# Performance work log

Hardware: AMD Instinct MI355X
Metric: run time of the kernel (lower is better)

Reference implementation:

```python
import jax, jax.numpy as jnp
import numpy as np

QUERY_DIM = 256
HIDDEN_DIM = 256
NUM_HEADS = 8
HEAD_DIM = HIDDEN_DIM // NUM_HEADS
NORM_FACT = float(HIDDEN_DIM / NUM_HEADS) ** (-0.5)


def setup_inputs() -> dict:
    key = jax.random.key(0)
    ks = jax.random.split(key, 7)
    b, Q, H, W = 4, 300, 100, 100
    q = jax.random.normal(ks[0], (b, Q, QUERY_DIM), dtype=jnp.float32)
    k = jax.random.normal(ks[1], (b, QUERY_DIM, H, W), dtype=jnp.float32)
    mask = jax.random.randint(ks[2], (b, H, W), 0, 2).astype(jnp.bool_)
    # xavier_uniform for Linear(query_dim, hidden_dim): bound = sqrt(6/(fan_in+fan_out))
    bound = float(np.sqrt(6.0 / (QUERY_DIM + HIDDEN_DIM)))
    q_w = jax.random.uniform(ks[3], (HIDDEN_DIM, QUERY_DIM), jnp.float32, -bound, bound)
    k_w = jax.random.uniform(ks[4], (HIDDEN_DIM, QUERY_DIM), jnp.float32, -bound, bound)
    q_b = jnp.zeros((HIDDEN_DIM,), jnp.float32)
    k_b = jnp.zeros((HIDDEN_DIM,), jnp.float32)
    return {"q": q, "k": k, "mask": mask, "q_w": q_w, "q_b": q_b, "k_w": k_w, "k_b": k_b}


def reference(q, k, mask, q_w, q_b, k_w, k_b):
    b, Q, _ = q.shape
    _, C, H, W = k.shape
    # q_linear: [b,Q,query_dim] -> [b,Q,hidden]
    qp = jnp.einsum('bqc,hc->bqh', q, q_w) + q_b
    # k projection: 1x1 conv == channel-wise linear: [b,C,H,W] -> [b,hidden,H,W]
    kp = jnp.einsum('bchw,oc->bohw', k, k_w) + k_b[None, :, None, None]
    qh = qp.reshape(b, Q, NUM_HEADS, HEAD_DIM)
    kh = kp.reshape(b, NUM_HEADS, HEAD_DIM, H, W)
    # attention scores: [b, Q, n_heads, H, W]
    weights = jnp.einsum('bqnc,bnchw->bqnhw', qh * NORM_FACT, kh)
    if mask is not None:
        weights = jnp.where(mask[:, None, None, :, :], -jnp.inf, weights)
    # softmax over flattened (heads, H, W) — faithful to flatten(2) in the original
    flat = weights.reshape(b, Q, NUM_HEADS * H * W)
    weights = jax.nn.softmax(flat, axis=-1).reshape(b, Q, NUM_HEADS, H, W)
    return weights
```

## Files before the change

### kernel.cpp

```cpp
#include <hip/hip_runtime.h>
#include <math.h>

#define BB 4
#define QQ 300
#define CC 256
#define NH 8
#define HD 32
#define HWN 10000
#define NT 625
#define NCHUNK 125
#define TPC 5
#define MT 19
#define NORM_FACT 0.17677669529663687f

typedef __attribute__((ext_vector_type(8))) short short8_t;
typedef __attribute__((ext_vector_type(4))) float f32x4_t;
typedef __attribute__((ext_vector_type(4))) int   i32x4_t;

union FragU { uint32_t u[4]; short8_t v; };

__device__ __forceinline__ unsigned short bf16_rn(float x) {
    uint32_t u = __float_as_uint(x);
    return (unsigned short)((u + 0x7fffu + ((u >> 16) & 1u)) >> 16);
}
__device__ __forceinline__ float bf16_f(unsigned short h) {
    return __uint_as_float(((uint32_t)h) << 16);
}

__global__ void prep_kwB_kernel(const float* __restrict__ kw,
                                unsigned short* __restrict__ kwB_hi,
                                unsigned short* __restrict__ kwB_lo) {
    const int ot = blockIdx.x, ks = blockIdx.y;
    const int l = threadIdx.x;
    const int o = ot * 16 + (l & 15);
    const int c0 = ks * 32 + (l >> 4) * 8;
    const size_t base = ((size_t)(ot * 8 + ks) * 64 + l) * 8;
    #pragma unroll
    for (int j = 0; j < 8; ++j) {
        const float x = kw[o * CC + c0 + j];
        const unsigned short h = bf16_rn(x);
        kwB_hi[base + j] = h;
        kwB_lo[base + j] = bf16_rn(x - bf16_f(h));
    }
}

__global__ void qproj_kernel(const float* __restrict__ q,
                             const float* __restrict__ qw,
                             const float* __restrict__ qb,
                             unsigned short* __restrict__ qp_il) {
    __shared__ float qrow[CC];
    const int bq = blockIdx.x;
    const int h  = threadIdx.x;
    qrow[h] = q[bq * CC + h];
    __syncthreads();
    float acc = qb[h];
    const float* wr = qw + h * CC;
    #pragma unroll 4
    for (int c = 0; c < CC; c += 4) {
        float4 w = *reinterpret_cast<const float4*>(wr + c);
        float4 x = *reinterpret_cast<const float4*>(&qrow[c]);
        acc += w.x * x.x + w.y * x.y + w.z * x.z + w.w * x.w;
    }
    acc *= NORM_FACT;
    const unsigned short hi = bf16_rn(acc);
    const size_t base = ((size_t)bq * NH + (h >> 5)) * 64 + (h & 31);
    qp_il[base]      = hi;
    qp_il[base + 32] = bf16_rn(acc - bf16_f(hi));
}

__global__ __launch_bounds__(256)
void kproj_kernel(const float* __restrict__ kin,
                  const unsigned short* __restrict__ kwB_hi,
                  const unsigned short* __restrict__ kwB_lo,
                  const float* __restrict__ kb,
                  unsigned short* __restrict__ kp_il) {
    const int wid = threadIdx.x >> 6, l = threadIdx.x & 63;
    const int wu  = blockIdx.x * 4 + wid;
    const int ot4 = wu & 3;
    const int rem = wu >> 2;
    const int hwt = rem % NT;
    const int b   = rem / NT;
    const int hw  = hwt * 16 + (l & 15);
    const int jb  = (l >> 4) * 8;

    f32x4_t acc[4];
    #pragma unroll
    for (int t = 0; t < 4; ++t) {
        const float bias = kb[(ot4 * 4 + t) * 16 + (l & 15)];
        acc[t] = {bias, bias, bias, bias};
    }

    const float* kbase = kin + (size_t)b * CC * HWN + hw;
    #pragma unroll 2
    for (int ks = 0; ks < 8; ++ks) {
        FragU a_hi, a_lo;
        #pragma unroll
        for (int tt = 0; tt < 4; ++tt) {
            const int c = ks * 32 + jb + 2 * tt;
            const float x0 = kbase[(size_t)c * HWN];
            const float x1 = kbase[(size_t)(c + 1) * HWN];
            const unsigned short h0 = bf16_rn(x0), h1 = bf16_rn(x1);
            const unsigned short g0 = bf16_rn(x0 - bf16_f(h0));
            const unsigned short g1 = bf16_rn(x1 - bf16_f(h1));
            a_hi.u[tt] = (uint32_t)h0 | ((uint32_t)h1 << 16);
            a_lo.u[tt] = (uint32_t)g0 | ((uint32_t)g1 << 16);
        }
        #pragma unroll
        for (int t = 0; t < 4; ++t) {
            const int ot = ot4 * 4 + t;
            const size_t fb = ((size_t)(ot * 8 + ks) * 64 + l) * 8;
            const short8_t bh = *reinterpret_cast<const short8_t*>(kwB_hi + fb);
            const short8_t bl = *reinterpret_cast<const short8_t*>(kwB_lo + fb);
            acc[t] = __builtin_amdgcn_mfma_f32_16x16x32_bf16(a_hi.v, bh, acc[t], 0, 0, 0);
            acc[t] = __builtin_amdgcn_mfma_f32_16x16x32_bf16(a_hi.v, bl, acc[t], 0, 0, 0);
            acc[t] = __builtin_amdgcn_mfma_f32_16x16x32_bf16(a_lo.v, bh, acc[t], 0, 0, 0);
        }
    }

    #pragma unroll
    for (int t = 0; t < 4; ++t) {
        const int o = (ot4 * 4 + t) * 16 + (l & 15);
        const int n = o >> 5, osub = o & 31;
        #pragma unroll
        for (int r = 0; r < 4; ++r) {
            const int hwrow = hwt * 16 + (l >> 4) * 4 + r;
            const size_t base = ((size_t)(b * HWN + hwrow) * NH + n) * 64 + osub;
            const float v = acc[t][r];
            const unsigned short h = bf16_rn(v);
            kp_il[base]      = h;
            kp_il[base + 32] = bf16_rn(v - bf16_f(h));
        }
    }
}

__global__ __launch_bounds__(256)
void attn_stats_kernel(const unsigned short* __restrict__ qp_il,
                       const unsigned short* __restrict__ kp_il,
                       const int* __restrict__ mask,
                       float* __restrict__ partials) {
    const int wid = threadIdx.x >> 6, l = threadIdx.x & 63;
    const int wu = blockIdx.x * 4 + wid;
    const int ch = wu % NCHUNK;
    int tmp = wu / NCHUNK;
    const int n = tmp & 7;
    const int b = tmp >> 3;

    short8_t ah[TPC], al[TPC];
    float mf[TPC][4];
    #pragma unroll
    for (int t = 0; t < TPC; ++t) {
        const int tile = ch * TPC + t;
        const int hwr = tile * 16 + (l & 15);
        const size_t abase = ((size_t)(b * HWN + hwr) * NH + n) * 64 + (l >> 4) * 8;
        ah[t] = *reinterpret_cast<const short8_t*>(kp_il + abase);
        al[t] = *reinterpret_cast<const short8_t*>(kp_il + abase + 32);
        const int hw4 = tile * 16 + (l >> 4) * 4;
        const i32x4_t mv = *reinterpret_cast<const i32x4_t*>(mask + b * HWN + hw4);
        mf[t][0] = mv.x ? 0.f : 1.f;
        mf[t][1] = mv.y ? 0.f : 1.f;
        mf[t][2] = mv.z ? 0.f : 1.f;
        mf[t][3] = mv.w ? 0.f : 1.f;
    }

    const size_t qslice = ((size_t)b * QQ) * NH + n;
    #pragma unroll 2
    for (int qt = 0; qt < MT; ++qt) {
        const int qa = qt * 16 + (l & 15);
        const int qcl = qa < QQ ? qa : QQ - 1;
        const size_t bbase = ((size_t)(b * QQ + qcl) * NH + n) * 64 + (l >> 4) * 8;
        const short8_t bh = *reinterpret_cast<const short8_t*>(qp_il + bbase);
        const short8_t bl = *reinterpret_cast<const short8_t*>(qp_il + bbase + 32);

        float a = 0.f;
        #pragma unroll
        for (int t = 0; t < TPC; ++t) {
            f32x4_t c = {0.f, 0.f, 0.f, 0.f};
            c = __builtin_amdgcn_mfma_f32_16x16x32_bf16(ah[t], bh, c, 0, 0, 0);
            c = __builtin_amdgcn_mfma_f32_16x16x32_bf16(ah[t], bl, c, 0, 0, 0);
            c = __builtin_amdgcn_mfma_f32_16x16x32_bf16(al[t], bh, c, 0, 0, 0);
            a += __expf(c[0]) * mf[t][0] + __expf(c[1]) * mf[t][1]
               + __expf(c[2]) * mf[t][2] + __expf(c[3]) * mf[t][3];
        }
        a += __shfl_xor(a, 16, 64);
        a += __shfl_xor(a, 32, 64);
        if (l < 16) {
            const int qr = qt * 16 + l;
            if (qr < QQ)
                partials[(((size_t)b * QQ + qr) * NH + n) * NCHUNK + ch] = a;
        }
    }
    (void)qslice;
}

__global__ void invsum_kernel(const float* __restrict__ partials,
                              float* __restrict__ invS) {
    const int row = blockIdx.x;
    const int l = threadIdx.x;
    float s = 0.f;
    const float* p = partials + (size_t)row * (NH * NCHUNK);
    for (int i = l; i < NH * NCHUNK; i += 64) s += p[i];
    #pragma unroll
    for (int m = 1; m < 64; m <<= 1) s += __shfl_xor(s, m, 64);
    if (l == 0) invS[row] = 1.0f / s;
}

__global__ __launch_bounds__(256)
void attn_out_kernel(const unsigned short* __restrict__ qp_il,
                     const unsigned short* __restrict__ kp_il,
                     const int* __restrict__ mask,
                     const float* __restrict__ invS,
                     float* __restrict__ out) {
    const int wid = threadIdx.x >> 6, l = threadIdx.x & 63;
    const int wu = blockIdx.x * 4 + wid;
    const int ch = wu % NCHUNK;
    int tmp = wu / NCHUNK;
    const int n = tmp & 7;
    const int b = tmp >> 3;

    short8_t ah[TPC], al[TPC];
    float mf[TPC][4];
    int hw4v[TPC];
    #pragma unroll
    for (int t = 0; t < TPC; ++t) {
        const int tile = ch * TPC + t;
        const int hwr = tile * 16 + (l & 15);
        const size_t abase = ((size_t)(b * HWN + hwr) * NH + n) * 64 + (l >> 4) * 8;
        ah[t] = *reinterpret_cast<const short8_t*>(kp_il + abase);
        al[t] = *reinterpret_cast<const short8_t*>(kp_il + abase + 32);
        const int hw4 = tile * 16 + (l >> 4) * 4;
        hw4v[t] = hw4;
        const i32x4_t mv = *reinterpret_cast<const i32x4_t*>(mask + b * HWN + hw4);
        mf[t][0] = mv.x ? 0.f : 1.f;
        mf[t][1] = mv.y ? 0.f : 1.f;
        mf[t][2] = mv.z ? 0.f : 1.f;
        mf[t][3] = mv.w ? 0.f : 1.f;
    }

    #pragma unroll 2
    for (int qt = 0; qt < MT; ++qt) {
        const int qa = qt * 16 + (l & 15);
        const int qcl = qa < QQ ? qa : QQ - 1;
        const bool qok = qa < QQ;
        const size_t bbase = ((size_t)(b * QQ + qcl) * NH + n) * 64 + (l >> 4) * 8;
        const short8_t bh = *reinterpret_cast<const short8_t*>(qp_il + bbase);
        const short8_t bl = *reinterpret_cast<const short8_t*>(qp_il + bbase + 32);
        const float is = invS[b * QQ + qcl];
        float* const obase = out + (((size_t)b * QQ + qcl) * NH + n) * HWN;

        #pragma unroll
        for (int t = 0; t < TPC; ++t) {
            f32x4_t c = {0.f, 0.f, 0.f, 0.f};
            c = __builtin_amdgcn_mfma_f32_16x16x32_bf16(ah[t], bh, c, 0, 0, 0);
            c = __builtin_amdgcn_mfma_f32_16x16x32_bf16(ah[t], bl, c, 0, 0, 0);
            c = __builtin_amdgcn_mfma_f32_16x16x32_bf16(al[t], bh, c, 0, 0, 0);
            f32x4_t rv;
            rv[0] = __expf(c[0]) * is * mf[t][0];
            rv[1] = __expf(c[1]) * is * mf[t][1];
            rv[2] = __expf(c[2]) * is * mf[t][2];
            rv[3] = __expf(c[3]) * is * mf[t][3];
            if (qok)
                __builtin_nontemporal_store(rv,
                    reinterpret_cast<f32x4_t*>(obase + hw4v[t]));
        }
    }
}

extern "C" void kernel_launch(void* const* d_in, const int* in_sizes, int n_in,
                              void* d_out, int out_size, void* d_ws, size_t ws_size,
                              hipStream_t stream) {
    const float* q    = (const float*)d_in[0];
    const float* k    = (const float*)d_in[1];
    const int*   mask = (const int*)d_in[2];
    const float* qw   = (const float*)d_in[3];
    const float* qb   = (const float*)d_in[4];
    const float* kw   = (const float*)d_in[5];
    const float* kb   = (const float*)d_in[6];
    float* out = (float*)d_out;

    char* wsb = (char*)d_ws;
    unsigned short* kp_il = (unsigned short*)wsb;
    unsigned short* qp_il = (unsigned short*)(wsb + 40960000);
    float* invS           = (float*)(wsb + 40960000 + 1228800);

    unsigned short* kwB_hi = (unsigned short*)d_out;
    unsigned short* kwB_lo = kwB_hi + 65536;
    float* partials = (float*)((char*)d_out + (4u << 20));

    prep_kwB_kernel<<<dim3(16, 8), 64, 0, stream>>>(kw, kwB_hi, kwB_lo);
    qproj_kernel<<<BB * QQ, 256, 0, stream>>>(q, qw, qb, qp_il);
    kproj_kernel<<<(BB * NT * 4) / 4, 256, 0, stream>>>(k, kwB_hi, kwB_lo, kb, kp_il);
    attn_stats_kernel<<<(BB * NH * NCHUNK) / 4, 256, 0, stream>>>(
        qp_il, kp_il, mask, partials);
    invsum_kernel<<<BB * QQ, 64, 0, stream>>>(partials, invS);
    attn_out_kernel<<<(BB * NH * NCHUNK) / 4, 256, 0, stream>>>(
        qp_il, kp_il, mask, invS, out);
}
```

Baseline: 249.0 us.

## Stage k tile in shared memory for kproj and split Q tiles across two waves

```diff
diff --git a/kernel.cpp b/kernel.cpp
--- a/kernel.cpp
+++ b/kernel.cpp
@@ -74,31 +74,48 @@
                   const unsigned short* __restrict__ kwB_lo,
                   const float* __restrict__ kb,
                   unsigned short* __restrict__ kp_il) {
+    __shared__ float kf[CC][17];
     const int wid = threadIdx.x >> 6, l = threadIdx.x & 63;
-    const int wu  = blockIdx.x * 4 + wid;
-    const int ot4 = wu & 3;
-    const int rem = wu >> 2;
-    const int hwt = rem % NT;
-    const int b   = rem / NT;
-    const int hw  = hwt * 16 + (l & 15);
+    const int bu  = blockIdx.x;
+    const int hwt = bu % NT;
+    const int b   = bu / NT;
+    const int ot4 = wid;
+
+    {
+        const int tid = threadIdx.x;
+        const float* kb0 = kin + (size_t)b * CC * HWN + hwt * 16;
+        #pragma unroll
+        for (int iter = 0; iter < 4; ++iter) {
+            const int c   = iter * 64 + (tid >> 2);
+            const int col = (tid & 3) * 4;
+            const float4 v = *reinterpret_cast<const float4*>(
+                kb0 + (size_t)c * HWN + col);
+            kf[c][col]     = v.x;
+            kf[c][col + 1] = v.y;
+            kf[c][col + 2] = v.z;
+            kf[c][col + 3] = v.w;
+        }
+    }
+    __syncthreads();
+
     const int jb  = (l >> 4) * 8;
+    const int col = l & 15;
 
     f32x4_t acc[4];
     #pragma unroll
     for (int t = 0; t < 4; ++t) {
-        const float bias = kb[(ot4 * 4 + t) * 16 + (l & 15)];
+        const float bias = kb[(ot4 * 4 + t) * 16 + col];
         acc[t] = {bias, bias, bias, bias};
     }
 
-    const float* kbase = kin + (size_t)b * CC * HWN + hw;
     #pragma unroll 2
     for (int ks = 0; ks < 8; ++ks) {
         FragU a_hi, a_lo;
         #pragma unroll
         for (int tt = 0; tt < 4; ++tt) {
             const int c = ks * 32 + jb + 2 * tt;
-            const float x0 = kbase[(size_t)c * HWN];
-            const float x1 = kbase[(size_t)(c + 1) * HWN];
+            const float x0 = kf[c][col];
+            const float x1 = kf[c + 1][col];
             const unsigned short h0 = bf16_rn(x0), h1 = bf16_rn(x1);
             const unsigned short g0 = bf16_rn(x0 - bf16_f(h0));
             const unsigned short g1 = bf16_rn(x1 - bf16_f(h1));
@@ -119,7 +136,7 @@
 
     #pragma unroll
     for (int t = 0; t < 4; ++t) {
-        const int o = (ot4 * 4 + t) * 16 + (l & 15);
+        const int o = (ot4 * 4 + t) * 16 + col;
         const int n = o >> 5, osub = o & 31;
         #pragma unroll
         for (int r = 0; r < 4; ++r) {
@@ -140,8 +157,9 @@
                        float* __restrict__ partials) {
     const int wid = threadIdx.x >> 6, l = threadIdx.x & 63;
     const int wu = blockIdx.x * 4 + wid;
-    const int ch = wu % NCHUNK;
-    int tmp = wu / NCHUNK;
+    const int qh = wu & 1;
+    int tmp = wu >> 1;
+    const int ch = tmp % NCHUNK; tmp /= NCHUNK;
     const int n = tmp & 7;
     const int b = tmp >> 3;
 
@@ -162,9 +180,10 @@
         mf[t][3] = mv.w ? 0.f : 1.f;
     }
 
-    const size_t qslice = ((size_t)b * QQ) * NH + n;
+    const int qt0 = qh * 10;
+    const int qt1 = qh ? MT : 10;
     #pragma unroll 2
-    for (int qt = 0; qt < MT; ++qt) {
+    for (int qt = qt0; qt < qt1; ++qt) {
         const int qa = qt * 16 + (l & 15);
         const int qcl = qa < QQ ? qa : QQ - 1;
         const size_t bbase = ((size_t)(b * QQ + qcl) * NH + n) * 64 + (l >> 4) * 8;
@@ -189,7 +208,6 @@
                 partials[(((size_t)b * QQ + qr) * NH + n) * NCHUNK + ch] = a;
         }
     }
-    (void)qslice;
 }
 
 __global__ void invsum_kernel(const float* __restrict__ partials,
@@ -212,8 +230,9 @@
                      float* __restrict__ out) {
     const int wid = threadIdx.x >> 6, l = threadIdx.x & 63;
     const int wu = blockIdx.x * 4 + wid;
-    const int ch = wu % NCHUNK;
-    int tmp = wu / NCHUNK;
+    const int qh = wu & 1;
+    int tmp = wu >> 1;
+    const int ch = tmp % NCHUNK; tmp /= NCHUNK;
     const int n = tmp & 7;
     const int b = tmp >> 3;
 
@@ -236,8 +255,10 @@
         mf[t][3] = mv.w ? 0.f : 1.f;
     }
 
+    const int qt0 = qh * 10;
+    const int qt1 = qh ? MT : 10;
     #pragma unroll 2
-    for (int qt = 0; qt < MT; ++qt) {
+    for (int qt = qt0; qt < qt1; ++qt) {
         const int qa = qt * 16 + (l & 15);
         const int qcl = qa < QQ ? qa : QQ - 1;
         const bool qok = qa < QQ;
@@ -288,10 +309,10 @@
 
     prep_kwB_kernel<<<dim3(16, 8), 64, 0, stream>>>(kw, kwB_hi, kwB_lo);
     qproj_kernel<<<BB * QQ, 256, 0, stream>>>(q, qw, qb, qp_il);
-    kproj_kernel<<<(BB * NT * 4) / 4, 256, 0, stream>>>(k, kwB_hi, kwB_lo, kb, kp_il);
-    attn_stats_kernel<<<(BB * NH * NCHUNK) / 4, 256, 0, stream>>>(
+    kproj_kernel<<<BB * NT, 256, 0, stream>>>(k, kwB_hi, kwB_lo, kb, kp_il);
+    attn_stats_kernel<<<(BB * NH * NCHUNK * 2) / 4, 256, 0, stream>>>(
         qp_il, kp_il, mask, partials);
     invsum_kernel<<<BB * QQ, 64, 0, stream>>>(partials, invS);
-    attn_out_kernel<<<(BB * NH * NCHUNK) / 4, 256, 0, stream>>>(
+    attn_out_kernel<<<(BB * NH * NCHUNK * 2) / 4, 256, 0, stream>>>(
         qp_il, kp_il, mask, invS, out);
 }
```

New measurement: 251.6 us. About the same (+1.1%).
